# Kernel optimization log

Hardware: AMD Instinct MI355X
Metric: run time of the kernel (lower is better)

## Reference

```python
import jax, jax.numpy as jnp
import numpy as np
from jax import lax

K_GROUPS = 4
CH = 256
CG = CH // K_GROUPS  # 64
KK = 9  # 3x3 kernel taps


def setup_inputs() -> dict:
    key = jax.random.key(0)
    ks = jax.random.split(key, 4)
    x = jax.random.normal(ks[0], (16, CH, 64, 64), dtype=jnp.float32)
    # offset-predicting conv: Cg -> 18 (2 offsets per 3x3 tap); small init so offsets are modest
    off_w = jax.random.normal(ks[1], (K_GROUPS, 18, CG, 3, 3), dtype=jnp.float32) * 0.01
    off_b = jnp.zeros((K_GROUPS, 18), dtype=jnp.float32)
    # deformable conv weights: Cg -> Cg, 3x3
    def_w = jax.random.normal(ks[2], (K_GROUPS, CG, CG, 3, 3), dtype=jnp.float32) * (1.0 / np.sqrt(CG * KK))
    def_b = jnp.zeros((K_GROUPS, CG), dtype=jnp.float32)
    return {"x": x, "off_w": off_w, "off_b": off_b, "def_w": def_w, "def_b": def_b}


def _bilinear_sample(img, py, px):
    # img: [B,Cg,H,W]; py,px: [B,KK,H,W] float sample coords -> [B,Cg,KK,H,W]
    B, C, H, W = img.shape
    K = py.shape[1]
    imgf = img.reshape(B, C, H * W)
    y0 = jnp.floor(py)
    x0 = jnp.floor(px)
    wy = py - y0
    wx = px - x0

    def gather(yi, xi, wgt):
        valid = (yi >= 0) & (yi < H) & (xi >= 0) & (xi < W)  # zero padding outside
        yc = jnp.clip(yi, 0, H - 1).astype(jnp.int32)
        xc = jnp.clip(xi, 0, W - 1).astype(jnp.int32)
        idx = (yc * W + xc).reshape(B, 1, K * H * W)
        v = jnp.take_along_axis(imgf, idx, axis=2).reshape(B, C, K, H, W)
        w = (wgt * valid.astype(img.dtype)).reshape(B, 1, K, H, W)
        return v * w

    return (gather(y0, x0, (1 - wy) * (1 - wx))
            + gather(y0, x0 + 1, (1 - wy) * wx)
            + gather(y0 + 1, x0, wy * (1 - wx))
            + gather(y0 + 1, x0 + 1, wy * wx))


def _group_forward(xg, ow, ob, dw, db):
    # xg: [B,Cg,H,W]
    B, C, H, W = xg.shape
    offset = lax.conv_general_dilated(xg, ow, (1, 1), ((1, 1), (1, 1)),
                                      dimension_numbers=("NCHW", "OIHW", "NCHW"))
    offset = offset + ob[None, :, None, None]            # [B,18,H,W]
    off = offset.reshape(B, KK, 2, H, W)                  # per-tap (dy,dx)
    ky, kx = jnp.meshgrid(jnp.arange(-1, 2), jnp.arange(-1, 2), indexing="ij")
    ky = ky.reshape(KK).astype(xg.dtype)
    kx = kx.reshape(KK).astype(xg.dtype)
    hh = jnp.arange(H, dtype=xg.dtype)
    ww = jnp.arange(W, dtype=xg.dtype)
    py = off[:, :, 0] + ky[None, :, None, None] + hh[None, None, :, None]  # [B,KK,H,W]
    px = off[:, :, 1] + kx[None, :, None, None] + ww[None, None, None, :]
    sampled = _bilinear_sample(xg, py, px)                # [B,Cg,KK,H,W]
    out = jnp.einsum("oik,bikhw->bohw", dw.reshape(dw.shape[0], dw.shape[1], KK), sampled)
    return out + db[None, :, None, None]


def reference(x, off_w, off_b, def_w, def_b):
    xs = jnp.split(x, K_GROUPS, axis=1)  # mirrors torch.split over channel groups
    outs = [_group_forward(xs[g], off_w[g], off_b[g], def_w[g], def_b[g])
            for g in range(K_GROUPS)]
    return jnp.concatenate(outs, axis=1)
```

## Files before the change

kernel.cpp:

```cpp
#include <hip/hip_runtime.h>
#include <hip/hip_bf16.h>
#include <hip/hip_fp16.h>

#define B_  16
#define G_  4
#define CG  64
#define H_  64
#define W_  64
#define KK  9
#define HW  (H_ * W_)
#define IP  72
#define PD  68
#define XSLICE (PD * PD * CG)

typedef short    short8  __attribute__((ext_vector_type(8)));
typedef _Float16 half8   __attribute__((ext_vector_type(8)));
typedef _Float16 h2      __attribute__((ext_vector_type(2)));
typedef float    f32x4   __attribute__((ext_vector_type(4)));
typedef float    f32x16  __attribute__((ext_vector_type(16)));

__device__ __forceinline__ short f2h(float v) {
    _Float16 h = (_Float16)v;
    short s;
    __builtin_memcpy(&s, &h, 2);
    return s;
}

__device__ __forceinline__ unsigned int pk2h(float a, float b) {
    h2 h = { (_Float16)a, (_Float16)b };
    unsigned int u;
    __builtin_memcpy(&u, &h, 4);
    return u;
}

__device__ __forceinline__ unsigned int interp2h(unsigned int c00, unsigned int c01,
                                                 unsigned int c10, unsigned int c11,
                                                 h2 w00, h2 w01, h2 w10, h2 w11) {
    h2 v00, v01, v10, v11;
    __builtin_memcpy(&v00, &c00, 4);
    __builtin_memcpy(&v01, &c01, 4);
    __builtin_memcpy(&v10, &c10, 4);
    __builtin_memcpy(&v11, &c11, 4);
    h2 r = v00 * w00 + v01 * w01 + v10 * w10 + v11 * w11;
    unsigned int o;
    __builtin_memcpy(&o, &r, 4);
    return o;
}

__global__ __launch_bounds__(256)
void prep_all(const float* __restrict__ x,
              const float* __restrict__ off_w,
              const float* __restrict__ def_w,
              short* __restrict__ xTpad,
              short* __restrict__ dwA32,
              short* __restrict__ owA)
{
    const int blk = blockIdx.x;
    const int t   = threadIdx.x;

    if (blk < 1024) {
        const int bg = blk >> 4;
        const int y0 = (blk & 15) * 4;

        __shared__ unsigned int sBw[4 * CG * 33];

        const float* src = x + (size_t)bg * CG * HW + (size_t)y0 * W_;
        const int i  = t >> 2;
        const int x0 = (t & 3) * 16;

        float4 v[4][4];
#pragma unroll
        for (int r = 0; r < 4; r++) {
            const float* sp = src + (size_t)i * HW + r * W_ + x0;
#pragma unroll
            for (int c = 0; c < 4; c++) v[r][c] = ((const float4*)sp)[c];
        }

#pragma unroll
        for (int r = 0; r < 4; r++) {
#pragma unroll
            for (int c = 0; c < 4; c++) {
                const unsigned int u0 = pk2h(v[r][c].x, v[r][c].y);
                const unsigned int u1 = pk2h(v[r][c].z, v[r][c].w);
                const int base = (r * CG + i) * 33 + ((x0 + 4 * c) >> 1);
                sBw[base]     = u0;
                sBw[base + 1] = u1;
            }
        }
        __syncthreads();

        const short* sBs = (const short*)sBw;
        short* dst = xTpad + (size_t)bg * XSLICE;
#pragma unroll
        for (int r = 0; r < 4; r++) {
            const int yp = y0 + 2 + r;
            for (int task = t; task < PD * 8; task += 256) {
                const int ich = task & 7;
                const int xp  = task >> 3;
                const int xx  = xp - 2;
                short8 o = {0, 0, 0, 0, 0, 0, 0, 0};
                if ((unsigned)xx < (unsigned)W_) {
#pragma unroll
                    for (int e = 0; e < 8; e++)
                        o[e] = sBs[(r * CG + ich * 8 + e) * 66 + xx];
                }
                *(short8*)(dst + ((size_t)yp * PD + xp) * CG + ich * 8) = o;
            }
        }
        return;
    }

    if (blk < 1088) {
        const int bg = blk - 1024;
        short* dstb = xTpad + (size_t)bg * XSLICE;
        const int4 z = {0, 0, 0, 0};
        int4* d0 = (int4*)(dstb);
        int4* d1 = (int4*)(dstb + (size_t)66 * PD * CG);
        const int n16 = (2 * PD * CG * 2) / 16;
        for (int c = t; c < n16; c += 256) { d0[c] = z; d1[c] = z; }
        return;
    }

    const int tid = (blk - 1088) * 256 + t;
    const int ndw = G_ * KK * 4096;
    const int now = G_ * 18 * 2 * 4 * 16 * 8;
    if (tid < ndw) {
        const int e    = tid & 7;
        const int o    = (tid >> 3) & 31;
        const int q2   = (tid >> 8) & 1;
        const int step = (tid >> 9) & 3;
        const int mt   = (tid >> 11) & 1;
        const int gk   = tid >> 12;
        const int k    = gk % KK;
        const int g    = gk / KK;
        const int oo   = mt * 32 + o;
        const int i    = step * 16 + q2 * 8 + e;
        dwA32[tid] = f2h(def_w[((g * CG + oo) * CG + i) * KK + k]);
    } else if (tid < ndw + now) {
        const int t2 = tid - ndw;
        const int e  = t2 & 7;
        const int jj = (t2 >> 3) & 15;
        const int q  = (t2 >> 7) & 3;
        const int tm = (t2 >> 9) & 1;
        const int gs = t2 >> 10;
        const int s  = gs % 18;
        const int g  = gs / 18;
        const int j  = tm * 16 + jj;
        const int rc = s >> 1;
        const int i  = (s & 1) * 32 + q * 8 + e;
        owA[t2] = (j < 18) ? f2h(off_w[((g * 18 + j) * CG + i) * KK + rc]) : (short)0;
    }
}

__global__ __launch_bounds__(256, 4)
void deform_main(const short* __restrict__ xTpad,
                 const float* __restrict__ off_b,
                 const float* __restrict__ def_b,
                 const short* __restrict__ dwA32,
                 const short* __restrict__ owA,
                 float* __restrict__ out)
{
    const int raw = blockIdx.x;
    const int r8  = raw & 7;
    const int h   = (raw >> 3) & 63;
    const int q8  = raw >> 9;
    const int bg  = q8 * 8 + r8;
    const int b   = bg >> 2;
    const int g   = bg & 3;

    __shared__ float2 pcs[KK][64];
    __shared__ short  sPool[8704];

    short* sT = sPool;
    short* sW = sPool + 64 * IP;

    const int t    = threadIdx.x;
    const int lane = t & 63;
    const int p    = t >> 6;
    const int nn   = lane & 15;
    const int q    = lane >> 4;

    const short* xb = xTpad + (size_t)bg * XSLICE;

    {
        const short* owAg = owA + g * 18 * 1024;
        f32x4 oa0 = {0.f, 0.f, 0.f, 0.f};
        f32x4 oa1 = {0.f, 0.f, 0.f, 0.f};

        *(uint4*)&sW[(0 & 1) * 2048 + t * 8] = *(const uint4*)(owAg + t * 8);
        __syncthreads();
#pragma unroll
        for (int rc = 0; rc < 9; rc++) {
            const int rr = rc / 3;
            const int cc = rc % 3;
            if (rc < 8)
                *(uint4*)&sW[((rc + 1) & 1) * 2048 + t * 8] =
                    *(const uint4*)(owAg + (rc + 1) * 2048 + t * 8);
            const short* cp = xb + ((h + rr + 1) * PD + (p * 16 + nn + cc + 1)) * CG + q * 8;
            const half8 b0 = *(const half8*)cp;
            const half8 b1 = *(const half8*)(cp + 32);
            const short* aw = &sW[(rc & 1) * 2048];
            const half8 a00 = *(const half8*)(aw +        q * 128 + nn * 8);
            const half8 a01 = *(const half8*)(aw +  512 + q * 128 + nn * 8);
            const half8 a10 = *(const half8*)(aw + 1024 + q * 128 + nn * 8);
            const half8 a11 = *(const half8*)(aw + 1536 + q * 128 + nn * 8);
            oa0 = __builtin_amdgcn_mfma_f32_16x16x32_f16(a00, b0, oa0, 0, 0, 0);
            oa1 = __builtin_amdgcn_mfma_f32_16x16x32_f16(a01, b0, oa1, 0, 0, 0);
            oa0 = __builtin_amdgcn_mfma_f32_16x16x32_f16(a10, b1, oa0, 0, 0, 0);
            oa1 = __builtin_amdgcn_mfma_f32_16x16x32_f16(a11, b1, oa1, 0, 0, 0);
            __syncthreads();
        }
        const int n = p * 16 + nn;
#pragma unroll
        for (int reg = 0; reg < 4; reg++) {
            const int j  = q * 4 + reg;
            const int kk = j >> 1;
            const float v = oa0[reg] + off_b[g * 18 + j];
            if ((j & 1) == 0) pcs[kk][n].x = v + (float)(kk / 3) + (float)(h + 1);
            else              pcs[kk][n].y = v + (float)(kk % 3) + (float)(n + 1);
        }
        if (q == 0) {
            pcs[8][n].x = oa1[0] + off_b[g * 18 + 16] + 2.0f + (float)(h + 1);
            pcs[8][n].y = oa1[1] + off_b[g * 18 + 17] + 2.0f + (float)(n + 1);
        }
    }

    const int mt  = p >> 1;
    const int nt  = p & 1;
    const int n31 = lane & 31;
    const int q2  = lane >> 5;

    f32x16 acc = {0.f};
    const short* dwg = dwA32 + g * KK * 4096;

    const int posL  = lane >> 3;
    const int chidx = lane & 7;
    const int posA  = p * 16 + posL;
    const int posB  = posA + 8;

    uint4 ca00, ca01, ca10, ca11;
    uint4 cb00, cb01, cb10, cb11;
    float wya, wxa, wyb, wxb;

    auto issue_g = [&](int k) {
        {
            const float2 pc = pcs[k][posA];
            const float yf = floorf(pc.x);
            const float xf = floorf(pc.y);
            wya = pc.x - yf;
            wxa = pc.y - xf;
            int y0 = (int)yf;
            int x0 = (int)xf;
            y0 = (y0 < 0) ? 0 : ((y0 > 66) ? 66 : y0);
            x0 = (x0 < 0) ? 0 : ((x0 > 66) ? 66 : x0);
            const short* cp = xb + (y0 * PD + x0) * CG + chidx * 8;
            ca00 = *(const uint4*)cp;
            ca01 = *(const uint4*)(cp + CG);
            ca10 = *(const uint4*)(cp + PD * CG);
            ca11 = *(const uint4*)(cp + PD * CG + CG);
        }
        {
            const float2 pc = pcs[k][posB];
            const float yf = floorf(pc.x);
            const float xf = floorf(pc.y);
            wyb = pc.x - yf;
            wxb = pc.y - xf;
            int y0 = (int)yf;
            int x0 = (int)xf;
            y0 = (y0 < 0) ? 0 : ((y0 > 66) ? 66 : y0);
            x0 = (x0 < 0) ? 0 : ((x0 > 66) ? 66 : x0);
            const short* cp = xb + (y0 * PD + x0) * CG + chidx * 8;
            cb00 = *(const uint4*)cp;
            cb01 = *(const uint4*)(cp + CG);
            cb10 = *(const uint4*)(cp + PD * CG);
            cb11 = *(const uint4*)(cp + PD * CG + CG);
        }
    };

    auto write_t = [&]() {
        {
            const float a00 = (1.0f - wya) * (1.0f - wxa);
            const float a01 = (1.0f - wya) * wxa;
            const float a10 = wya * (1.0f - wxa);
            const float a11 = wya * wxa;
            const h2 w00 = { (_Float16)a00, (_Float16)a00 };
            const h2 w01 = { (_Float16)a01, (_Float16)a01 };
            const h2 w10 = { (_Float16)a10, (_Float16)a10 };
            const h2 w11 = { (_Float16)a11, (_Float16)a11 };
            uint4 ov;
            ov.x = interp2h(ca00.x, ca01.x, ca10.x, ca11.x, w00, w01, w10, w11);
            ov.y = interp2h(ca00.y, ca01.y, ca10.y, ca11.y, w00, w01, w10, w11);
            ov.z = interp2h(ca00.z, ca01.z, ca10.z, ca11.z, w00, w01, w10, w11);
            ov.w = interp2h(ca00.w, ca01.w, ca10.w, ca11.w, w00, w01, w10, w11);
            *(uint4*)&sT[posA * IP + chidx * 8] = ov;
        }
        {
            const float a00 = (1.0f - wyb) * (1.0f - wxb);
            const float a01 = (1.0f - wyb) * wxb;
            const float a10 = wyb * (1.0f - wxb);
            const float a11 = wyb * wxb;
            const h2 w00 = { (_Float16)a00, (_Float16)a00 };
            const h2 w01 = { (_Float16)a01, (_Float16)a01 };
            const h2 w10 = { (_Float16)a10, (_Float16)a10 };
            const h2 w11 = { (_Float16)a11, (_Float16)a11 };
            uint4 ov;
            ov.x = interp2h(cb00.x, cb01.x, cb10.x, cb11.x, w00, w01, w10, w11);
            ov.y = interp2h(cb00.y, cb01.y, cb10.y, cb11.y, w00, w01, w10, w11);
            ov.z = interp2h(cb00.z, cb01.z, cb10.z, cb11.z, w00, w01, w10, w11);
            ov.w = interp2h(cb00.w, cb01.w, cb10.w, cb11.w, w00, w01, w10, w11);
            *(uint4*)&sT[posB * IP + chidx * 8] = ov;
        }
    };

    auto stage_af = [&](int k) {
        const short* dwk = dwg + k * 4096;
        *(uint4*)&sW[t * 8]        = *(const uint4*)(dwk + t * 8);
        *(uint4*)&sW[2048 + t * 8] = *(const uint4*)(dwk + 2048 + t * 8);
    };

    auto einsum_t = [&]() {
        const half8 af0 = *(const half8*)&sW[((mt * 4 + 0) * 2 + q2) * 256 + n31 * 8];
        const half8 af1 = *(const half8*)&sW[((mt * 4 + 1) * 2 + q2) * 256 + n31 * 8];
        const half8 af2 = *(const half8*)&sW[((mt * 4 + 2) * 2 + q2) * 256 + n31 * 8];
        const half8 af3 = *(const half8*)&sW[((mt * 4 + 3) * 2 + q2) * 256 + n31 * 8];
        const half8 bf0 = *(const half8*)&sT[(nt * 32 + n31) * IP + 0 * 16 + q2 * 8];
        const half8 bf1 = *(const half8*)&sT[(nt * 32 + n31) * IP + 1 * 16 + q2 * 8];
        const half8 bf2 = *(const half8*)&sT[(nt * 32 + n31) * IP + 2 * 16 + q2 * 8];
        const half8 bf3 = *(const half8*)&sT[(nt * 32 + n31) * IP + 3 * 16 + q2 * 8];
        acc = __builtin_amdgcn_mfma_f32_32x32x16_f16(af0, bf0, acc, 0, 0, 0);
        acc = __builtin_amdgcn_mfma_f32_32x32x16_f16(af1, bf1, acc, 0, 0, 0);
        acc = __builtin_amdgcn_mfma_f32_32x32x16_f16(af2, bf2, acc, 0, 0, 0);
        acc = __builtin_amdgcn_mfma_f32_32x32x16_f16(af3, bf3, acc, 0, 0, 0);
    };

    stage_af(0);
    issue_g(0);
    write_t();
    __syncthreads();
#pragma unroll
    for (int k = 0; k < KK; k++) {
        if (k < KK - 1) issue_g(k + 1);
        einsum_t();
        if (k < KK - 1) {
            __syncthreads();
            write_t();
            stage_af(k + 1);
            __syncthreads();
        }
    }

    __syncthreads();
    float* eT = (float*)sPool;
    {
        const int n = nt * 32 + n31;
#pragma unroll
        for (int reg = 0; reg < 16; reg++) {
            const int o = mt * 32 + (reg & 3) + 8 * (reg >> 2) + 4 * q2;
            eT[o * 65 + n] = acc[reg];
        }
    }
    __syncthreads();
    {
        const int row = t >> 2;
        const int c4  = (t & 3) * 4;
        const float bias = def_b[g * 64 + row];
        float* outp = out + (size_t)(b * 256 + g * 64) * HW + h * W_ + (size_t)row * HW;
        const float* e = &eT[row * 65];
#pragma unroll
        for (int j0 = 0; j0 < 4; j0++) {
            const int c = c4 + j0 * 16;
            float4 r;
            r.x = e[c + 0] + bias;
            r.y = e[c + 1] + bias;
            r.z = e[c + 2] + bias;
            r.w = e[c + 3] + bias;
            *(float4*)&outp[c] = r;
        }
    }
}

__global__ __launch_bounds__(256, 4)
void deform_fallback(const float* __restrict__ x,
                     const float* __restrict__ off_w,
                     const float* __restrict__ off_b,
                     const float* __restrict__ def_w,
                     const float* __restrict__ def_b,
                     float* __restrict__ out)
{
    const int raw = blockIdx.x;
    const int r8  = raw & 7;
    const int h   = (raw >> 3) & 63;
    const int q8  = raw >> 9;
    const int bg  = q8 * 8 + r8;
    const int b   = bg >> 2;
    const int g   = bg & 3;

    __shared__ float pys[KK][W_];
    __shared__ float pxs[KK][W_];
    __shared__ float buf[8192];
    float* red   = buf;
    float* s_lds = buf;
    float* dwTl  = buf + 4096;

    const int t = threadIdx.x;
    const int w = t & 63;
    const int p = t >> 6;

    const float* xg = x + (size_t)(b * 256 + g * 64) * HW;

    float acc[18];
#pragma unroll
    for (int j = 0; j < 18; j++) acc[j] = 0.0f;
    {
        const int i0 = p * 16;
        for (int ii = 0; ii < 16; ii++) {
            const int i = i0 + ii;
            const float* xi = xg + i * HW;
#pragma unroll
            for (int r = 0; r < 3; r++) {
                const int y = h + r - 1;
                if ((unsigned)y >= (unsigned)H_) continue;
#pragma unroll
                for (int c = 0; c < 3; c++) {
                    const int xc = w + c - 1;
                    const float xv = ((unsigned)xc < (unsigned)W_) ? xi[y * W_ + xc] : 0.0f;
#pragma unroll
                    for (int j = 0; j < 18; j++) {
                        const float wv = off_w[((g * 18 + j) * CG + i) * 9 + r * 3 + c];
                        acc[j] = fmaf(wv, xv, acc[j]);
                    }
                }
            }
        }
    }
#pragma unroll
    for (int j = 0; j < 18; j++) red[(p * 18 + j) * 64 + w] = acc[j];
    __syncthreads();
    for (int idx = t; idx < 18 * 64; idx += 256) {
        const int j  = idx >> 6;
        const int ww = idx & 63;
        float v = red[(0 * 18 + j) * 64 + ww] + red[(1 * 18 + j) * 64 + ww]
                + red[(2 * 18 + j) * 64 + ww] + red[(3 * 18 + j) * 64 + ww];
        v += off_b[g * 18 + j];
        const int k = j >> 1;
        if ((j & 1) == 0) pys[k][ww] = v + (float)(k / 3 - 1) + (float)h;
        else              pxs[k][ww] = v + (float)(k % 3 - 1) + (float)ww;
    }
    __syncthreads();

    float facc[16];
#pragma unroll
    for (int qd = 0; qd < 16; qd++) facc[qd] = 0.0f;
    const int w4 = (t & 15) << 2;
    const int o4 = (t >> 4) << 2;

    for (int k = 0; k < KK; k++) {
#pragma unroll
        for (int n = 0; n < 16; n++) {
            const int v = t + 256 * n;
            const int i = v >> 6;
            const int o = v & 63;
            dwTl[v] = def_w[((g * CG + o) * CG + i) * KK + k];
        }
        const float py  = pys[k][w];
        const float px  = pxs[k][w];
        const float y0f = floorf(py);
        const float x0f = floorf(px);
        const float wy  = py - y0f;
        const float wx  = px - x0f;
        const int   y0  = (int)y0f;
        const int   x0  = (int)x0f;
        const float w00 = (1.0f - wy) * (1.0f - wx);
        const float w01 = (1.0f - wy) * wx;
        const float w10 = wy * (1.0f - wx);
        const float w11 = wy * wx;
        const bool vy0 = (unsigned)y0       < (unsigned)H_;
        const bool vy1 = (unsigned)(y0 + 1) < (unsigned)H_;
        const bool vx0 = (unsigned)x0       < (unsigned)W_;
        const bool vx1 = (unsigned)(x0 + 1) < (unsigned)W_;
        const int a00 = y0 * W_ + x0;
#pragma unroll
        for (int n = 0; n < 16; n++) {
            const int i = (n << 2) + p;
            const float* xi = xg + i * HW;
            const float v00 = (vy0 && vx0) ? xi[a00]          : 0.0f;
            const float v01 = (vy0 && vx1) ? xi[a00 + 1]      : 0.0f;
            const float v10 = (vy1 && vx0) ? xi[a00 + W_]     : 0.0f;
            const float v11 = (vy1 && vx1) ? xi[a00 + W_ + 1] : 0.0f;
            s_lds[i * 64 + w] = w00 * v00 + w01 * v01 + w10 * v10 + w11 * v11;
        }
        __syncthreads();
#pragma unroll 4
        for (int i = 0; i < CG; i++) {
            const float4 sv = *(const float4*)&s_lds[i * 64 + w4];
            const float4 dv = *(const float4*)&dwTl[i * 64 + o4];
            facc[0]  = fmaf(dv.x, sv.x, facc[0]);
            facc[1]  = fmaf(dv.x, sv.y, facc[1]);
            facc[2]  = fmaf(dv.x, sv.z, facc[2]);
            facc[3]  = fmaf(dv.x, sv.w, facc[3]);
            facc[4]  = fmaf(dv.y, sv.x, facc[4]);
            facc[5]  = fmaf(dv.y, sv.y, facc[5]);
            facc[6]  = fmaf(dv.y, sv.z, facc[6]);
            facc[7]  = fmaf(dv.y, sv.w, facc[7]);
            facc[8]  = fmaf(dv.z, sv.x, facc[8]);
            facc[9]  = fmaf(dv.z, sv.y, facc[9]);
            facc[10] = fmaf(dv.z, sv.z, facc[10]);
            facc[11] = fmaf(dv.z, sv.w, facc[11]);
            facc[12] = fmaf(dv.w, sv.x, facc[12]);
            facc[13] = fmaf(dv.w, sv.y, facc[13]);
            facc[14] = fmaf(dv.w, sv.z, facc[14]);
            facc[15] = fmaf(dv.w, sv.w, facc[15]);
        }
        __syncthreads();
    }

    float* outp = out + (size_t)(b * 256 + g * 64) * HW + h * W_;
#pragma unroll
    for (int oo = 0; oo < 4; oo++) {
        const int o = o4 + oo;
        const float bias = def_b[g * 64 + o];
        float4 r;
        r.x = facc[oo * 4 + 0] + bias;
        r.y = facc[oo * 4 + 1] + bias;
        r.z = facc[oo * 4 + 2] + bias;
        r.w = facc[oo * 4 + 3] + bias;
        *(float4*)&outp[o * HW + w4] = r;
    }
}

extern "C" void kernel_launch(void* const* d_in, const int* in_sizes, int n_in,
                              void* d_out, int out_size, void* d_ws, size_t ws_size,
                              hipStream_t stream)
{
    (void)in_sizes; (void)n_in; (void)out_size;
    const float* x     = (const float*)d_in[0];
    const float* off_w = (const float*)d_in[1];
    const float* off_b = (const float*)d_in[2];
    const float* def_w = (const float*)d_in[3];
    const float* def_b = (const float*)d_in[4];
    float* out = (float*)d_out;

    const size_t xT_bytes  = (size_t)B_ * G_ * XSLICE * 2;
    const size_t dw_bytes  = (size_t)G_ * KK * 4096 * 2;
    const size_t ow_bytes  = (size_t)G_ * 18 * 1024 * 2;
    const size_t need = xT_bytes + dw_bytes + ow_bytes;

    const int nblk   = B_ * G_ * H_;
    const int nprepw = (G_ * KK * 4096 + G_ * 18 * 1024 + 255) / 256;
    const int nprep  = 1024 + 64 + nprepw;

    if (ws_size >= need) {
        short* xTpad = (short*)d_ws;
        short* dwA32 = (short*)((char*)d_ws + xT_bytes);
        short* owA   = (short*)((char*)d_ws + xT_bytes + dw_bytes);
        prep_all<<<nprep, 256, 0, stream>>>(x, off_w, def_w, xTpad, dwA32, owA);
        deform_main<<<nblk, 256, 0, stream>>>(xTpad, off_b, def_b, dwA32, owA, out);
    } else {
        deform_fallback<<<nblk, 256, 0, stream>>>(x, off_w, off_b, def_w, def_b, out);
    }
}
```

Baseline: 201.1 us.

## Process two output rows per 512-thread block sharing staged weights

```diff
diff --git a/kernel.cpp b/kernel.cpp
--- a/kernel.cpp
+++ b/kernel.cpp
@@ -152,7 +152,7 @@
     }
 }
 
-__global__ __launch_bounds__(256, 4)
+__global__ __launch_bounds__(512, 4)
 void deform_main(const short* __restrict__ xTpad,
                  const float* __restrict__ off_b,
                  const float* __restrict__ def_b,
@@ -162,23 +162,26 @@
 {
     const int raw = blockIdx.x;
     const int r8  = raw & 7;
-    const int h   = (raw >> 3) & 63;
-    const int q8  = raw >> 9;
+    const int hh  = (raw >> 3) & 31;
+    const int q8  = raw >> 8;
     const int bg  = q8 * 8 + r8;
     const int b   = bg >> 2;
     const int g   = bg & 3;
 
-    __shared__ float2 pcs[KK][64];
-    __shared__ short  sPool[8704];
-
-    short* sT = sPool;
-    short* sW = sPool + 64 * IP;
+    __shared__ __align__(16) char smem[35840];
 
     const int t    = threadIdx.x;
-    const int lane = t & 63;
-    const int p    = t >> 6;
+    const int grp  = t >> 8;
+    const int tg   = t & 255;
+    const int h    = hh * 2 + grp;
+    const int lane = tg & 63;
+    const int p    = tg >> 6;
     const int nn   = lane & 15;
     const int q    = lane >> 4;
+
+    float2 (*pcsg)[64] = (float2 (*)[64])(smem + grp * 4608);
+    short* sT = (short*)(smem + 9216) + grp * (64 * IP);
+    short* sW = (short*)(smem + 27648);
 
     const short* xb = xTpad + (size_t)bg * XSLICE;
 
@@ -187,13 +190,13 @@
         f32x4 oa0 = {0.f, 0.f, 0.f, 0.f};
         f32x4 oa1 = {0.f, 0.f, 0.f, 0.f};
 
-        *(uint4*)&sW[(0 & 1) * 2048 + t * 8] = *(const uint4*)(owAg + t * 8);
+        if (t < 256) *(uint4*)&sW[t * 8] = *(const uint4*)(owAg + t * 8);
         __syncthreads();
 #pragma unroll
         for (int rc = 0; rc < 9; rc++) {
             const int rr = rc / 3;
             const int cc = rc % 3;
-            if (rc < 8)
+            if (rc < 8 && t < 256)
                 *(uint4*)&sW[((rc + 1) & 1) * 2048 + t * 8] =
                     *(const uint4*)(owAg + (rc + 1) * 2048 + t * 8);
             const short* cp = xb + ((h + rr + 1) * PD + (p * 16 + nn + cc + 1)) * CG + q * 8;
@@ -216,12 +219,12 @@
             const int j  = q * 4 + reg;
             const int kk = j >> 1;
             const float v = oa0[reg] + off_b[g * 18 + j];
-            if ((j & 1) == 0) pcs[kk][n].x = v + (float)(kk / 3) + (float)(h + 1);
-            else              pcs[kk][n].y = v + (float)(kk % 3) + (float)(n + 1);
+            if ((j & 1) == 0) pcsg[kk][n].x = v + (float)(kk / 3) + (float)(h + 1);
+            else              pcsg[kk][n].y = v + (float)(kk % 3) + (float)(n + 1);
         }
         if (q == 0) {
-            pcs[8][n].x = oa1[0] + off_b[g * 18 + 16] + 2.0f + (float)(h + 1);
-            pcs[8][n].y = oa1[1] + off_b[g * 18 + 17] + 2.0f + (float)(n + 1);
+            pcsg[8][n].x = oa1[0] + off_b[g * 18 + 16] + 2.0f + (float)(h + 1);
+            pcsg[8][n].y = oa1[1] + off_b[g * 18 + 17] + 2.0f + (float)(n + 1);
         }
     }
 
@@ -244,7 +247,7 @@
 
     auto issue_g = [&](int k) {
         {
-            const float2 pc = pcs[k][posA];
+            const float2 pc = pcsg[k][posA];
             const float yf = floorf(pc.x);
             const float xf = floorf(pc.y);
             wya = pc.x - yf;
@@ -260,7 +263,7 @@
             ca11 = *(const uint4*)(cp + PD * CG + CG);
         }
         {
-            const float2 pc = pcs[k][posB];
+            const float2 pc = pcsg[k][posB];
             const float yf = floorf(pc.x);
             const float xf = floorf(pc.y);
             wyb = pc.x - yf;
@@ -314,8 +317,7 @@
 
     auto stage_af = [&](int k) {
         const short* dwk = dwg + k * 4096;
-        *(uint4*)&sW[t * 8]        = *(const uint4*)(dwk + t * 8);
-        *(uint4*)&sW[2048 + t * 8] = *(const uint4*)(dwk + 2048 + t * 8);
+        *(uint4*)&sW[t * 8] = *(const uint4*)(dwk + t * 8);
     };
 
     auto einsum_t = [&]() {
@@ -350,7 +352,7 @@
     }
 
     __syncthreads();
-    float* eT = (float*)sPool;
+    float* eT = (float*)(smem + grp * 16640);
     {
         const int n = nt * 32 + n31;
 #pragma unroll
@@ -361,8 +363,8 @@
     }
     __syncthreads();
     {
-        const int row = t >> 2;
-        const int c4  = (t & 3) * 4;
+        const int row = tg >> 2;
+        const int c4  = (tg & 3) * 4;
         const float bias = def_b[g * 64 + row];
         float* outp = out + (size_t)(b * 256 + g * 64) * HW + h * W_ + (size_t)row * HW;
         const float* e = &eT[row * 65];
@@ -545,7 +547,7 @@
     const size_t ow_bytes  = (size_t)G_ * 18 * 1024 * 2;
     const size_t need = xT_bytes + dw_bytes + ow_bytes;
 
-    const int nblk   = B_ * G_ * H_;
+    const int nblk   = B_ * G_ * 32;
     const int nprepw = (G_ * KK * 4096 + G_ * 18 * 1024 + 255) / 256;
     const int nprep  = 1024 + 64 + nprepw;
 
@@ -554,8 +556,8 @@
         short* dwA32 = (short*)((char*)d_ws + xT_bytes);
         short* owA   = (short*)((char*)d_ws + xT_bytes + dw_bytes);
         prep_all<<<nprep, 256, 0, stream>>>(x, off_w, def_w, xTpad, dwA32, owA);
-        deform_main<<<nblk, 256, 0, stream>>>(xTpad, off_b, def_b, dwA32, owA, out);
+        deform_main<<<nblk, 512, 0, stream>>>(xTpad, off_b, def_b, dwA32, owA, out);
     } else {
-        deform_fallback<<<nblk, 256, 0, stream>>>(x, off_w, off_b, def_w, def_b, out);
-    }
-}
+        deform_fallback<<<B_ * G_ * H_, 256, 0, stream>>>(x, off_w, off_b, def_w, def_b, out);
+    }
+}
```

Result: slower. 206.1 us (+2.5%).
